# Performance work log

Hardware: AMD Instinct MI355X
Metric: run time of the kernel (lower is better)

Reference implementation:

```python
import jax, jax.numpy as jnp
import numpy as np

RANK = 16
ALPHA = 32
SCALING = ALPHA / RANK  # 2.0


def setup_inputs() -> dict:
    key = jax.random.key(0)
    k1, k2, k3 = jax.random.split(key, 3)
    B_, S, D, O = 2, 4096, 4096, 4096
    x = jax.random.normal(k1, (B_, S, D), dtype=jnp.float32)
    # Dequantized base weight, torch Linear layout [out, in]
    W_base = jax.random.normal(k2, (O, D), dtype=jnp.float32) * 0.02
    # kaiming_uniform-ish init for lora_A [rank, in]
    bound = float(np.sqrt(6.0 / (1 + 5) / D))
    A = jax.random.uniform(k3, (RANK, D), dtype=jnp.float32, minval=-bound, maxval=bound)
    # lora_B initialized to zeros [out, rank]
    Bm = jnp.zeros((O, RANK), dtype=jnp.float32)
    return {"x": x, "W_base": W_base, "A": A, "B": Bm}


def reference(x, W_base, A, B):
    # Y = x @ W_base^T + (x @ A^T) @ B^T * scaling   (dropout p=0 -> identity)
    base_out = jnp.einsum('bsd,od->bso', x, W_base)
    lora_mid = jnp.einsum('bsd,rd->bsr', x, A)        # [B,S,rank]
    lora_out = jnp.einsum('bsr,or->bso', lora_mid, B) # [B,S,out]
    return base_out + lora_out * SCALING
```

## Files before the change

kernel.cpp:

```cpp
#include <hip/hip_runtime.h>
#include <hip/hip_bf16.h>

typedef __attribute__((ext_vector_type(8))) __bf16 bf16x8;
typedef __attribute__((ext_vector_type(4))) float  f32x4;

__global__ __launch_bounds__(256) void cvt_f32_bf16(
    const float* __restrict__ in, __bf16* __restrict__ out, long n8)
{
    long i = (long)blockIdx.x * blockDim.x + threadIdx.x;
    long stride = (long)gridDim.x * blockDim.x;
    for (; i < n8; i += stride) {
        const f32x4* p = (const f32x4*)(in + i * 8);
        f32x4 a = p[0], b = p[1];
        bf16x8 o;
        o[0] = (__bf16)a[0]; o[1] = (__bf16)a[1];
        o[2] = (__bf16)a[2]; o[3] = (__bf16)a[3];
        o[4] = (__bf16)b[0]; o[5] = (__bf16)b[1];
        o[6] = (__bf16)b[2]; o[7] = (__bf16)b[3];
        *(bf16x8*)(out + i * 8) = o;
    }
}

__global__ __launch_bounds__(256) void mid_and_cvt(
    const float* __restrict__ x, const float* __restrict__ A,
    float* __restrict__ mid, __bf16* __restrict__ Xb, int K)
{
    int m = blockIdx.x;
    int tid = threadIdx.x;
    const float* xr = x + (size_t)m * K;

    float acc[16];
#pragma unroll
    for (int r = 0; r < 16; ++r) acc[r] = 0.f;

    int iters = K / 2048;
    for (int it = 0; it < iters; ++it) {
        int k = it * 2048 + tid * 8;
        f32x4 x0 = *(const f32x4*)(xr + k);
        f32x4 x1 = *(const f32x4*)(xr + k + 4);
        if (Xb) {
            bf16x8 o;
            o[0] = (__bf16)x0[0]; o[1] = (__bf16)x0[1];
            o[2] = (__bf16)x0[2]; o[3] = (__bf16)x0[3];
            o[4] = (__bf16)x1[0]; o[5] = (__bf16)x1[1];
            o[6] = (__bf16)x1[2]; o[7] = (__bf16)x1[3];
            *(bf16x8*)(Xb + (size_t)m * K + k) = o;
        }
#pragma unroll
        for (int r = 0; r < 16; ++r) {
            const f32x4* ap = (const f32x4*)(A + (size_t)r * K + k);
            f32x4 a0 = ap[0], a1 = ap[1];
            acc[r] += x0[0]*a0[0] + x0[1]*a0[1] + x0[2]*a0[2] + x0[3]*a0[3]
                    + x1[0]*a1[0] + x1[1]*a1[1] + x1[2]*a1[2] + x1[3]*a1[3];
        }
    }

#pragma unroll
    for (int r = 0; r < 16; ++r) {
#pragma unroll
        for (int off = 32; off > 0; off >>= 1)
            acc[r] += __shfl_down(acc[r], off, 64);
    }
    __shared__ float red[4][16];
    int lane = tid & 63, w = tid >> 6;
    if (lane == 0) {
#pragma unroll
        for (int r = 0; r < 16; ++r) red[w][r] = acc[r];
    }
    __syncthreads();
    if (tid < 16) {
        float s = red[0][tid] + red[1][tid] + red[2][tid] + red[3][tid];
        mid[(size_t)m * 16 + tid] = s;
    }
}

#define GL16(g, l) __builtin_amdgcn_global_load_lds( \
    (const __attribute__((address_space(1))) void*)(g), \
    (__attribute__((address_space(3))) void*)(l), 16, 0, 0)

__global__ __launch_bounds__(512, 2) void gemm256(
    const __bf16* __restrict__ Xb,
    const __bf16* __restrict__ Wb,
    const float*  __restrict__ mid,
    const float*  __restrict__ Bl,
    float* __restrict__ out,
    int M, int N, int K)
{
    __shared__ __bf16 As[4][256 * 32];
    __shared__ __bf16 Bs[4][256 * 32];

    const int NT = K >> 5;

    int nbx = N >> 8, nby = M >> 8, nwg = nbx * nby;
    int bid = blockIdx.x, swz = bid;
    if ((nwg & 7) == 0) { int cpx = nwg >> 3; swz = (bid & 7) * cpx + (bid >> 3); }
    int by = swz / nbx, bx = swz % nbx;
    int m0 = by << 8, n0 = bx << 8;

    int tid = threadIdx.x;
    int lane = tid & 63;
    int w = tid >> 6;
    int wm = w >> 2, wn = w & 3;

    int q0 = tid >> 2;
    int c0 = tid & 3;
    int csrc = c0 ^ ((q0 >> 1) & 3);
    const __bf16* sA0 = Xb + (size_t)(m0 + q0) * K + csrc * 8;
    const __bf16* sA1 = sA0 + (size_t)128 * K;
    const __bf16* sB0 = Wb + (size_t)(n0 + q0) * K + csrc * 8;
    const __bf16* sB1 = sB0 + (size_t)128 * K;
    unsigned ldsw = (unsigned)w * 1024;

    int chunkSwz = (lane >> 4) ^ ((lane >> 1) & 3);
    unsigned aoff = (unsigned)((wm * 128 + (lane & 15)) * 64 + chunkSwz * 16);
    unsigned boff = (unsigned)((wn * 64  + (lane & 15)) * 64 + chunkSwz * 16);

    f32x4 acc[8][4];
    {
        int kh = lane >> 4;
        bf16x8 bI[4];
#pragma unroll
        for (int j = 0; j < 4; ++j) {
            bf16x8 v = {};
            if (kh < 2) {
                int col = n0 + wn * 64 + j * 16 + (lane & 15);
                const f32x4* p = (const f32x4*)(Bl + (size_t)col * 16 + kh * 8);
                f32x4 v0 = p[0], v1 = p[1];
                v[0] = (__bf16)(2.0f * v0[0]); v[1] = (__bf16)(2.0f * v0[1]);
                v[2] = (__bf16)(2.0f * v0[2]); v[3] = (__bf16)(2.0f * v0[3]);
                v[4] = (__bf16)(2.0f * v1[0]); v[5] = (__bf16)(2.0f * v1[1]);
                v[6] = (__bf16)(2.0f * v1[2]); v[7] = (__bf16)(2.0f * v1[3]);
            }
            bI[j] = v;
        }
#pragma unroll
        for (int i = 0; i < 8; ++i) {
            bf16x8 aI = {};
            if (kh < 2) {
                int row = m0 + wm * 128 + i * 16 + (lane & 15);
                const f32x4* p = (const f32x4*)(mid + (size_t)row * 16 + kh * 8);
                f32x4 v0 = p[0], v1 = p[1];
                aI[0] = (__bf16)v0[0]; aI[1] = (__bf16)v0[1];
                aI[2] = (__bf16)v0[2]; aI[3] = (__bf16)v0[3];
                aI[4] = (__bf16)v1[0]; aI[5] = (__bf16)v1[1];
                aI[6] = (__bf16)v1[2]; aI[7] = (__bf16)v1[3];
            }
            f32x4 z = {0.f, 0.f, 0.f, 0.f};
#pragma unroll
            for (int j = 0; j < 4; ++j)
                acc[i][j] = __builtin_amdgcn_mfma_f32_16x16x32_bf16(aI, bI[j], z, 0, 0, 0);
        }
    }

    {
        GL16(sA0, (char*)As[0] + ldsw);
        GL16(sA1, (char*)As[0] + 8192 + ldsw);
        GL16(sB0, (char*)Bs[0] + ldsw);
        GL16(sB1, (char*)Bs[0] + 8192 + ldsw);
        GL16(sA0 + 32, (char*)As[1] + ldsw);
        GL16(sA1 + 32, (char*)As[1] + 8192 + ldsw);
        GL16(sB0 + 32, (char*)Bs[1] + ldsw);
        GL16(sB1 + 32, (char*)Bs[1] + 8192 + ldsw);
    }
    asm volatile("s_waitcnt vmcnt(4)" ::: "memory");
    asm volatile("s_barrier" ::: "memory");

    int cur = 0;
    for (int t = 0; t < NT; ++t) {
        const __bf16* bufA = As[cur];
        const __bf16* bufB = Bs[cur];
        bool pf = (t + 2) < NT;
        int pb = (t + 2) & 3;
        size_t koff = (size_t)(t + 2) * 32;

        bf16x8 af0, af1, af2, af3, bf0, bf1, bf2, bf3;
        af0 = *(const bf16x8*)((const char*)bufA + aoff);
        af1 = *(const bf16x8*)((const char*)bufA + aoff + 1024);
        af2 = *(const bf16x8*)((const char*)bufA + aoff + 2048);
        af3 = *(const bf16x8*)((const char*)bufA + aoff + 3072);
        bf0 = *(const bf16x8*)((const char*)bufB + boff);
        bf1 = *(const bf16x8*)((const char*)bufB + boff + 1024);
        bf2 = *(const bf16x8*)((const char*)bufB + boff + 2048);
        bf3 = *(const bf16x8*)((const char*)bufB + boff + 3072);
        if (pf) {
            GL16(sA0 + koff, (char*)As[pb] + ldsw);
            GL16(sA1 + koff, (char*)As[pb] + 8192 + ldsw);
        }
        asm volatile("s_barrier" ::: "memory");
        asm volatile("s_waitcnt lgkmcnt(0)" ::: "memory");
        __builtin_amdgcn_sched_barrier(0);
        __builtin_amdgcn_s_setprio(1);
        acc[0][0] = __builtin_amdgcn_mfma_f32_16x16x32_bf16(af0, bf0, acc[0][0], 0, 0, 0);
        acc[0][1] = __builtin_amdgcn_mfma_f32_16x16x32_bf16(af0, bf1, acc[0][1], 0, 0, 0);
        acc[0][2] = __builtin_amdgcn_mfma_f32_16x16x32_bf16(af0, bf2, acc[0][2], 0, 0, 0);
        acc[0][3] = __builtin_amdgcn_mfma_f32_16x16x32_bf16(af0, bf3, acc[0][3], 0, 0, 0);
        acc[1][0] = __builtin_amdgcn_mfma_f32_16x16x32_bf16(af1, bf0, acc[1][0], 0, 0, 0);
        acc[1][1] = __builtin_amdgcn_mfma_f32_16x16x32_bf16(af1, bf1, acc[1][1], 0, 0, 0);
        acc[1][2] = __builtin_amdgcn_mfma_f32_16x16x32_bf16(af1, bf2, acc[1][2], 0, 0, 0);
        acc[1][3] = __builtin_amdgcn_mfma_f32_16x16x32_bf16(af1, bf3, acc[1][3], 0, 0, 0);
        acc[2][0] = __builtin_amdgcn_mfma_f32_16x16x32_bf16(af2, bf0, acc[2][0], 0, 0, 0);
        acc[2][1] = __builtin_amdgcn_mfma_f32_16x16x32_bf16(af2, bf1, acc[2][1], 0, 0, 0);
        acc[2][2] = __builtin_amdgcn_mfma_f32_16x16x32_bf16(af2, bf2, acc[2][2], 0, 0, 0);
        acc[2][3] = __builtin_amdgcn_mfma_f32_16x16x32_bf16(af2, bf3, acc[2][3], 0, 0, 0);
        acc[3][0] = __builtin_amdgcn_mfma_f32_16x16x32_bf16(af3, bf0, acc[3][0], 0, 0, 0);
        acc[3][1] = __builtin_amdgcn_mfma_f32_16x16x32_bf16(af3, bf1, acc[3][1], 0, 0, 0);
        acc[3][2] = __builtin_amdgcn_mfma_f32_16x16x32_bf16(af3, bf2, acc[3][2], 0, 0, 0);
        acc[3][3] = __builtin_amdgcn_mfma_f32_16x16x32_bf16(af3, bf3, acc[3][3], 0, 0, 0);
        __builtin_amdgcn_s_setprio(0);
        asm volatile("s_barrier" ::: "memory");

        af0 = *(const bf16x8*)((const char*)bufA + aoff + 4096);
        af1 = *(const bf16x8*)((const char*)bufA + aoff + 5120);
        af2 = *(const bf16x8*)((const char*)bufA + aoff + 6144);
        af3 = *(const bf16x8*)((const char*)bufA + aoff + 7168);
        if (pf) {
            GL16(sB0 + koff, (char*)Bs[pb] + ldsw);
            GL16(sB1 + koff, (char*)Bs[pb] + 8192 + ldsw);
        }
        asm volatile("s_barrier" ::: "memory");
        asm volatile("s_waitcnt lgkmcnt(0)" ::: "memory");
        __builtin_amdgcn_sched_barrier(0);
        __builtin_amdgcn_s_setprio(1);
        acc[4][0] = __builtin_amdgcn_mfma_f32_16x16x32_bf16(af0, bf0, acc[4][0], 0, 0, 0);
        acc[4][1] = __builtin_amdgcn_mfma_f32_16x16x32_bf16(af0, bf1, acc[4][1], 0, 0, 0);
        acc[4][2] = __builtin_amdgcn_mfma_f32_16x16x32_bf16(af0, bf2, acc[4][2], 0, 0, 0);
        acc[4][3] = __builtin_amdgcn_mfma_f32_16x16x32_bf16(af0, bf3, acc[4][3], 0, 0, 0);
        acc[5][0] = __builtin_amdgcn_mfma_f32_16x16x32_bf16(af1, bf0, acc[5][0], 0, 0, 0);
        acc[5][1] = __builtin_amdgcn_mfma_f32_16x16x32_bf16(af1, bf1, acc[5][1], 0, 0, 0);
        acc[5][2] = __builtin_amdgcn_mfma_f32_16x16x32_bf16(af1, bf2, acc[5][2], 0, 0, 0);
        acc[5][3] = __builtin_amdgcn_mfma_f32_16x16x32_bf16(af1, bf3, acc[5][3], 0, 0, 0);
        acc[6][0] = __builtin_amdgcn_mfma_f32_16x16x32_bf16(af2, bf0, acc[6][0], 0, 0, 0);
        acc[6][1] = __builtin_amdgcn_mfma_f32_16x16x32_bf16(af2, bf1, acc[6][1], 0, 0, 0);
        acc[6][2] = __builtin_amdgcn_mfma_f32_16x16x32_bf16(af2, bf2, acc[6][2], 0, 0, 0);
        acc[6][3] = __builtin_amdgcn_mfma_f32_16x16x32_bf16(af2, bf3, acc[6][3], 0, 0, 0);
        acc[7][0] = __builtin_amdgcn_mfma_f32_16x16x32_bf16(af3, bf0, acc[7][0], 0, 0, 0);
        acc[7][1] = __builtin_amdgcn_mfma_f32_16x16x32_bf16(af3, bf1, acc[7][1], 0, 0, 0);
        acc[7][2] = __builtin_amdgcn_mfma_f32_16x16x32_bf16(af3, bf2, acc[7][2], 0, 0, 0);
        acc[7][3] = __builtin_amdgcn_mfma_f32_16x16x32_bf16(af3, bf3, acc[7][3], 0, 0, 0);
        __builtin_amdgcn_s_setprio(0);
        if (pf) asm volatile("s_waitcnt vmcnt(4)" ::: "memory");
        else    asm volatile("s_waitcnt vmcnt(0)" ::: "memory");
        asm volatile("s_barrier" ::: "memory");

        cur = (cur + 1) & 3;
    }

#pragma unroll
    for (int i = 0; i < 8; ++i) {
        int rbase = m0 + wm * 128 + i * 16 + ((lane >> 4) << 2);
#pragma unroll
        for (int q = 0; q < 4; ++q) {
            float* orow = out + (size_t)(rbase + q) * N;
            int colb = n0 + wn * 64 + (lane & 15);
            orow[colb]      = acc[i][0][q];
            orow[colb + 16] = acc[i][1][q];
            orow[colb + 32] = acc[i][2][q];
            orow[colb + 48] = acc[i][3][q];
        }
    }
}

__global__ __launch_bounds__(256) void gemm_fb(
    const float* __restrict__ X, const float* __restrict__ W,
    const float* __restrict__ mid, const float* __restrict__ Bl,
    float* __restrict__ out, int M, int N, int K)
{
    __shared__ float As[64][16];
    __shared__ float Bs[64][16];
    int nbx = N / 64;
    int bx = blockIdx.x % nbx, by = blockIdx.x / nbx;
    int m0 = by * 64, n0 = bx * 64;
    int tid = threadIdx.x;
    int tr = tid >> 4, tc = tid & 15;

    float acc[4][4] = {};
    for (int kt = 0; kt < K; kt += 16) {
#pragma unroll
        for (int s = 0; s < 4; ++s) {
            int c = s * 256 + tid;
            int row = c >> 4, kk = c & 15;
            As[row][kk] = X[(size_t)(m0 + row) * K + kt + kk];
            Bs[row][kk] = W[(size_t)(n0 + row) * K + kt + kk];
        }
        __syncthreads();
#pragma unroll
        for (int kk = 0; kk < 16; ++kk) {
            float av[4], bv[4];
#pragma unroll
            for (int i = 0; i < 4; ++i) { av[i] = As[tr*4+i][kk]; bv[i] = Bs[tc*4+i][kk]; }
#pragma unroll
            for (int i = 0; i < 4; ++i)
#pragma unroll
                for (int j = 0; j < 4; ++j) acc[i][j] += av[i] * bv[j];
        }
        __syncthreads();
    }
#pragma unroll
    for (int i = 0; i < 4; ++i) {
        int row = m0 + tr * 4 + i;
#pragma unroll
        for (int j = 0; j < 4; ++j) {
            int col = n0 + tc * 4 + j;
            float s = 0.f;
#pragma unroll
            for (int r = 0; r < 16; ++r)
                s += mid[(size_t)row * 16 + r] * Bl[(size_t)col * 16 + r];
            out[(size_t)row * N + col] = acc[i][j] + 2.0f * s;
        }
    }
}

extern "C" void kernel_launch(void* const* d_in, const int* in_sizes, int n_in,
                              void* d_out, int out_size, void* d_ws, size_t ws_size,
                              hipStream_t stream)
{
    const float* x   = (const float*)d_in[0];
    const float* Wf  = (const float*)d_in[1];
    const float* A   = (const float*)d_in[2];
    const float* Bl  = (const float*)d_in[3];
    float* out = (float*)d_out;

    int D = in_sizes[2] / 16;
    int O = in_sizes[3] / 16;
    long M = (long)in_sizes[0] / D;
    int K = D, N = O;

    size_t xb_bytes  = (size_t)M * K * 2;
    size_t wb_bytes  = (size_t)N * K * 2;
    size_t mid_bytes = (size_t)M * 16 * 4;

    bool shapes_ok = (M % 256 == 0) && (N % 256 == 0) && (K % 32 == 0) && (K >= 128);

    if (shapes_ok && ws_size >= xb_bytes + wb_bytes + mid_bytes) {
        __bf16* Xb  = (__bf16*)d_ws;
        __bf16* Wbb = (__bf16*)((char*)d_ws + xb_bytes);
        float*  mid = (float*)((char*)d_ws + xb_bytes + wb_bytes);

        cvt_f32_bf16<<<2048, 256, 0, stream>>>(Wf, Wbb, (long)N * K / 8);
        mid_and_cvt<<<(int)M, 256, 0, stream>>>(x, A, mid, Xb, K);
        int nwg = (int)(M / 256) * (N / 256);
        gemm256<<<nwg, 512, 0, stream>>>(Xb, Wbb, mid, Bl, out, (int)M, N, K);
    } else {
        float* mid = (float*)d_ws;
        mid_and_cvt<<<(int)M, 256, 0, stream>>>(x, A, mid, nullptr, K);
        int nwg = (int)(M / 64) * (N / 64);
        gemm_fb<<<nwg, 256, 0, stream>>>(x, Wf, mid, Bl, out, (int)M, N, K);
    }
}
```

Measured before the change: 398.3 us.

## Process four rows per block in LoRA mid kernel and simplify GEMM k-loop

The LoRA projection kernel now handles four rows of x per block, so each load of A is reused across four rows and a quarter as many blocks are launched. The GEMM main loop drops its two-phase split, in which each half read fragments, synchronised with a barrier and waited on LDS. It now issues all prefetches first, loads all 8 A and 4 B fragments, and runs 32 MFMAs without intermediate barriers or sched_barrier. This lowers barrier overhead but raises register pressure and leaves LDS-wait placement to the compiler. The shape check now requires K to be a multiple of 2048.

```diff
diff --git a/kernel.cpp b/kernel.cpp
--- a/kernel.cpp
+++ b/kernel.cpp
@@ -23,54 +23,78 @@
 
 __global__ __launch_bounds__(256) void mid_and_cvt(
     const float* __restrict__ x, const float* __restrict__ A,
-    float* __restrict__ mid, __bf16* __restrict__ Xb, int K)
-{
-    int m = blockIdx.x;
+    float* __restrict__ mid, __bf16* __restrict__ Xb, int K, int M)
+{
     int tid = threadIdx.x;
-    const float* xr = x + (size_t)m * K;
-
-    float acc[16];
-#pragma unroll
-    for (int r = 0; r < 16; ++r) acc[r] = 0.f;
+    int m0 = blockIdx.x * 4;
+
+    float acc[4][16];
+#pragma unroll
+    for (int row = 0; row < 4; ++row)
+#pragma unroll
+        for (int r = 0; r < 16; ++r) acc[row][r] = 0.f;
 
     int iters = K / 2048;
     for (int it = 0; it < iters; ++it) {
         int k = it * 2048 + tid * 8;
-        f32x4 x0 = *(const f32x4*)(xr + k);
-        f32x4 x1 = *(const f32x4*)(xr + k + 4);
-        if (Xb) {
-            bf16x8 o;
-            o[0] = (__bf16)x0[0]; o[1] = (__bf16)x0[1];
-            o[2] = (__bf16)x0[2]; o[3] = (__bf16)x0[3];
-            o[4] = (__bf16)x1[0]; o[5] = (__bf16)x1[1];
-            o[6] = (__bf16)x1[2]; o[7] = (__bf16)x1[3];
-            *(bf16x8*)(Xb + (size_t)m * K + k) = o;
+        f32x4 xv[4][2];
+#pragma unroll
+        for (int row = 0; row < 4; ++row) {
+            if (m0 + row < M) {
+                const float* xr = x + (size_t)(m0 + row) * K;
+                xv[row][0] = *(const f32x4*)(xr + k);
+                xv[row][1] = *(const f32x4*)(xr + k + 4);
+            } else {
+                f32x4 z = {0.f,0.f,0.f,0.f};
+                xv[row][0] = z; xv[row][1] = z;
+            }
+            if (Xb && m0 + row < M) {
+                bf16x8 o;
+                o[0] = (__bf16)xv[row][0][0]; o[1] = (__bf16)xv[row][0][1];
+                o[2] = (__bf16)xv[row][0][2]; o[3] = (__bf16)xv[row][0][3];
+                o[4] = (__bf16)xv[row][1][0]; o[5] = (__bf16)xv[row][1][1];
+                o[6] = (__bf16)xv[row][1][2]; o[7] = (__bf16)xv[row][1][3];
+                *(bf16x8*)(Xb + (size_t)(m0 + row) * K + k) = o;
+            }
         }
 #pragma unroll
         for (int r = 0; r < 16; ++r) {
             const f32x4* ap = (const f32x4*)(A + (size_t)r * K + k);
             f32x4 a0 = ap[0], a1 = ap[1];
-            acc[r] += x0[0]*a0[0] + x0[1]*a0[1] + x0[2]*a0[2] + x0[3]*a0[3]
-                    + x1[0]*a1[0] + x1[1]*a1[1] + x1[2]*a1[2] + x1[3]*a1[3];
-        }
-    }
-
-#pragma unroll
-    for (int r = 0; r < 16; ++r) {
-#pragma unroll
-        for (int off = 32; off > 0; off >>= 1)
-            acc[r] += __shfl_down(acc[r], off, 64);
-    }
-    __shared__ float red[4][16];
+#pragma unroll
+            for (int row = 0; row < 4; ++row) {
+                acc[row][r] += xv[row][0][0]*a0[0] + xv[row][0][1]*a0[1]
+                             + xv[row][0][2]*a0[2] + xv[row][0][3]*a0[3]
+                             + xv[row][1][0]*a1[0] + xv[row][1][1]*a1[1]
+                             + xv[row][1][2]*a1[2] + xv[row][1][3]*a1[3];
+            }
+        }
+    }
+
+#pragma unroll
+    for (int row = 0; row < 4; ++row)
+#pragma unroll
+        for (int r = 0; r < 16; ++r)
+#pragma unroll
+            for (int off = 32; off > 0; off >>= 1)
+                acc[row][r] += __shfl_down(acc[row][r], off, 64);
+
+    __shared__ float red[4][4][16];
     int lane = tid & 63, w = tid >> 6;
     if (lane == 0) {
 #pragma unroll
-        for (int r = 0; r < 16; ++r) red[w][r] = acc[r];
+        for (int row = 0; row < 4; ++row)
+#pragma unroll
+            for (int r = 0; r < 16; ++r) red[w][row][r] = acc[row][r];
     }
     __syncthreads();
-    if (tid < 16) {
-        float s = red[0][tid] + red[1][tid] + red[2][tid] + red[3][tid];
-        mid[(size_t)m * 16 + tid] = s;
+    if (tid < 64) {
+        int row = tid >> 4, r = tid & 15;
+        if (m0 + row < M) {
+            float s = red[0][row][r] + red[1][row][r]
+                    + red[2][row][r] + red[3][row][r];
+            mid[(size_t)(m0 + row) * 16 + r] = s;
+        }
     }
 }
 
@@ -152,16 +176,14 @@
         }
     }
 
-    {
-        GL16(sA0, (char*)As[0] + ldsw);
-        GL16(sA1, (char*)As[0] + 8192 + ldsw);
-        GL16(sB0, (char*)Bs[0] + ldsw);
-        GL16(sB1, (char*)Bs[0] + 8192 + ldsw);
-        GL16(sA0 + 32, (char*)As[1] + ldsw);
-        GL16(sA1 + 32, (char*)As[1] + 8192 + ldsw);
-        GL16(sB0 + 32, (char*)Bs[1] + ldsw);
-        GL16(sB1 + 32, (char*)Bs[1] + 8192 + ldsw);
-    }
+    GL16(sA0, (char*)As[0] + ldsw);
+    GL16(sA1, (char*)As[0] + 8192 + ldsw);
+    GL16(sB0, (char*)Bs[0] + ldsw);
+    GL16(sB1, (char*)Bs[0] + 8192 + ldsw);
+    GL16(sA0 + 32, (char*)As[1] + ldsw);
+    GL16(sA1 + 32, (char*)As[1] + 8192 + ldsw);
+    GL16(sB0 + 32, (char*)Bs[1] + ldsw);
+    GL16(sB1 + 32, (char*)Bs[1] + 8192 + ldsw);
     asm volatile("s_waitcnt vmcnt(4)" ::: "memory");
     asm volatile("s_barrier" ::: "memory");
 
@@ -173,71 +195,30 @@
         int pb = (t + 2) & 3;
         size_t koff = (size_t)(t + 2) * 32;
 
-        bf16x8 af0, af1, af2, af3, bf0, bf1, bf2, bf3;
-        af0 = *(const bf16x8*)((const char*)bufA + aoff);
-        af1 = *(const bf16x8*)((const char*)bufA + aoff + 1024);
-        af2 = *(const bf16x8*)((const char*)bufA + aoff + 2048);
-        af3 = *(const bf16x8*)((const char*)bufA + aoff + 3072);
-        bf0 = *(const bf16x8*)((const char*)bufB + boff);
-        bf1 = *(const bf16x8*)((const char*)bufB + boff + 1024);
-        bf2 = *(const bf16x8*)((const char*)bufB + boff + 2048);
-        bf3 = *(const bf16x8*)((const char*)bufB + boff + 3072);
         if (pf) {
             GL16(sA0 + koff, (char*)As[pb] + ldsw);
             GL16(sA1 + koff, (char*)As[pb] + 8192 + ldsw);
-        }
-        asm volatile("s_barrier" ::: "memory");
-        asm volatile("s_waitcnt lgkmcnt(0)" ::: "memory");
-        __builtin_amdgcn_sched_barrier(0);
-        __builtin_amdgcn_s_setprio(1);
-        acc[0][0] = __builtin_amdgcn_mfma_f32_16x16x32_bf16(af0, bf0, acc[0][0], 0, 0, 0);
-        acc[0][1] = __builtin_amdgcn_mfma_f32_16x16x32_bf16(af0, bf1, acc[0][1], 0, 0, 0);
-        acc[0][2] = __builtin_amdgcn_mfma_f32_16x16x32_bf16(af0, bf2, acc[0][2], 0, 0, 0);
-        acc[0][3] = __builtin_amdgcn_mfma_f32_16x16x32_bf16(af0, bf3, acc[0][3], 0, 0, 0);
-        acc[1][0] = __builtin_amdgcn_mfma_f32_16x16x32_bf16(af1, bf0, acc[1][0], 0, 0, 0);
-        acc[1][1] = __builtin_amdgcn_mfma_f32_16x16x32_bf16(af1, bf1, acc[1][1], 0, 0, 0);
-        acc[1][2] = __builtin_amdgcn_mfma_f32_16x16x32_bf16(af1, bf2, acc[1][2], 0, 0, 0);
-        acc[1][3] = __builtin_amdgcn_mfma_f32_16x16x32_bf16(af1, bf3, acc[1][3], 0, 0, 0);
-        acc[2][0] = __builtin_amdgcn_mfma_f32_16x16x32_bf16(af2, bf0, acc[2][0], 0, 0, 0);
-        acc[2][1] = __builtin_amdgcn_mfma_f32_16x16x32_bf16(af2, bf1, acc[2][1], 0, 0, 0);
-        acc[2][2] = __builtin_amdgcn_mfma_f32_16x16x32_bf16(af2, bf2, acc[2][2], 0, 0, 0);
-        acc[2][3] = __builtin_amdgcn_mfma_f32_16x16x32_bf16(af2, bf3, acc[2][3], 0, 0, 0);
-        acc[3][0] = __builtin_amdgcn_mfma_f32_16x16x32_bf16(af3, bf0, acc[3][0], 0, 0, 0);
-        acc[3][1] = __builtin_amdgcn_mfma_f32_16x16x32_bf16(af3, bf1, acc[3][1], 0, 0, 0);
-        acc[3][2] = __builtin_amdgcn_mfma_f32_16x16x32_bf16(af3, bf2, acc[3][2], 0, 0, 0);
-        acc[3][3] = __builtin_amdgcn_mfma_f32_16x16x32_bf16(af3, bf3, acc[3][3], 0, 0, 0);
-        __builtin_amdgcn_s_setprio(0);
-        asm volatile("s_barrier" ::: "memory");
-
-        af0 = *(const bf16x8*)((const char*)bufA + aoff + 4096);
-        af1 = *(const bf16x8*)((const char*)bufA + aoff + 5120);
-        af2 = *(const bf16x8*)((const char*)bufA + aoff + 6144);
-        af3 = *(const bf16x8*)((const char*)bufA + aoff + 7168);
-        if (pf) {
             GL16(sB0 + koff, (char*)Bs[pb] + ldsw);
             GL16(sB1 + koff, (char*)Bs[pb] + 8192 + ldsw);
         }
-        asm volatile("s_barrier" ::: "memory");
-        asm volatile("s_waitcnt lgkmcnt(0)" ::: "memory");
-        __builtin_amdgcn_sched_barrier(0);
+
+        bf16x8 bfr[4], af[8];
+#pragma unroll
+        for (int j = 0; j < 4; ++j)
+            bfr[j] = *(const bf16x8*)((const char*)bufB + boff + j * 1024u);
+#pragma unroll
+        for (int i = 0; i < 8; ++i)
+            af[i] = *(const bf16x8*)((const char*)bufA + aoff + i * 1024u);
+
         __builtin_amdgcn_s_setprio(1);
-        acc[4][0] = __builtin_amdgcn_mfma_f32_16x16x32_bf16(af0, bf0, acc[4][0], 0, 0, 0);
-        acc[4][1] = __builtin_amdgcn_mfma_f32_16x16x32_bf16(af0, bf1, acc[4][1], 0, 0, 0);
-        acc[4][2] = __builtin_amdgcn_mfma_f32_16x16x32_bf16(af0, bf2, acc[4][2], 0, 0, 0);
-        acc[4][3] = __builtin_amdgcn_mfma_f32_16x16x32_bf16(af0, bf3, acc[4][3], 0, 0, 0);
-        acc[5][0] = __builtin_amdgcn_mfma_f32_16x16x32_bf16(af1, bf0, acc[5][0], 0, 0, 0);
-        acc[5][1] = __builtin_amdgcn_mfma_f32_16x16x32_bf16(af1, bf1, acc[5][1], 0, 0, 0);
-        acc[5][2] = __builtin_amdgcn_mfma_f32_16x16x32_bf16(af1, bf2, acc[5][2], 0, 0, 0);
-        acc[5][3] = __builtin_amdgcn_mfma_f32_16x16x32_bf16(af1, bf3, acc[5][3], 0, 0, 0);
-        acc[6][0] = __builtin_amdgcn_mfma_f32_16x16x32_bf16(af2, bf0, acc[6][0], 0, 0, 0);
-        acc[6][1] = __builtin_amdgcn_mfma_f32_16x16x32_bf16(af2, bf1, acc[6][1], 0, 0, 0);
-        acc[6][2] = __builtin_amdgcn_mfma_f32_16x16x32_bf16(af2, bf2, acc[6][2], 0, 0, 0);
-        acc[6][3] = __builtin_amdgcn_mfma_f32_16x16x32_bf16(af2, bf3, acc[6][3], 0, 0, 0);
-        acc[7][0] = __builtin_amdgcn_mfma_f32_16x16x32_bf16(af3, bf0, acc[7][0], 0, 0, 0);
-        acc[7][1] = __builtin_amdgcn_mfma_f32_16x16x32_bf16(af3, bf1, acc[7][1], 0, 0, 0);
-        acc[7][2] = __builtin_amdgcn_mfma_f32_16x16x32_bf16(af3, bf2, acc[7][2], 0, 0, 0);
-        acc[7][3] = __builtin_amdgcn_mfma_f32_16x16x32_bf16(af3, bf3, acc[7][3], 0, 0, 0);
+#pragma unroll
+        for (int i = 0; i < 8; ++i)
+#pragma unroll
+            for (int j = 0; j < 4; ++j)
+                acc[i][j] = __builtin_amdgcn_mfma_f32_16x16x32_bf16(
+                    af[i], bfr[j], acc[i][j], 0, 0, 0);
         __builtin_amdgcn_s_setprio(0);
+
         if (pf) asm volatile("s_waitcnt vmcnt(4)" ::: "memory");
         else    asm volatile("s_waitcnt vmcnt(0)" ::: "memory");
         asm volatile("s_barrier" ::: "memory");
@@ -329,7 +310,9 @@
     size_t wb_bytes  = (size_t)N * K * 2;
     size_t mid_bytes = (size_t)M * 16 * 4;
 
-    bool shapes_ok = (M % 256 == 0) && (N % 256 == 0) && (K % 32 == 0) && (K >= 128);
+    bool shapes_ok = (M % 256 == 0) && (N % 256 == 0) && (K % 2048 == 0);
+
+    int midgrid = (int)((M + 3) / 4);
 
     if (shapes_ok && ws_size >= xb_bytes + wb_bytes + mid_bytes) {
         __bf16* Xb  = (__bf16*)d_ws;
@@ -337,12 +320,12 @@
         float*  mid = (float*)((char*)d_ws + xb_bytes + wb_bytes);
 
         cvt_f32_bf16<<<2048, 256, 0, stream>>>(Wf, Wbb, (long)N * K / 8);
-        mid_and_cvt<<<(int)M, 256, 0, stream>>>(x, A, mid, Xb, K);
+        mid_and_cvt<<<midgrid, 256, 0, stream>>>(x, A, mid, Xb, K, (int)M);
         int nwg = (int)(M / 256) * (N / 256);
         gemm256<<<nwg, 512, 0, stream>>>(Xb, Wbb, mid, Bl, out, (int)M, N, K);
     } else {
         float* mid = (float*)d_ws;
-        mid_and_cvt<<<(int)M, 256, 0, stream>>>(x, A, mid, nullptr, K);
+        mid_and_cvt<<<midgrid, 256, 0, stream>>>(x, A, mid, nullptr, K, (int)M);
         int nwg = (int)(M / 64) * (N / 64);
         gemm_fb<<<nwg, 256, 0, stream>>>(x, Wf, mid, Bl, out, (int)M, N, K);
     }
```

After: 405.9 us. No clear change (+1.9%).
